# Performance work log

Hardware: AMD Instinct MI355X
Metric: run time of the kernel (lower is better)

The kernel has to match this reference:

```python
import jax, jax.numpy as jnp
import numpy as np

NINPUTS = 16
WIDTH = 128
KSIZE = 21
SPP = 8
BS, CI, H, W = 2, 3, 192, 192
EPS = 1e-08


def _conv(x, w, b, padding):
    y = jax.lax.conv_general_dilated(
        x, w, window_strides=(1, 1), padding=padding,
        dimension_numbers=("NCHW", "OIHW", "NCHW"))
    return y + b[None, :, None, None]


def apply_kernels(kernel, radiance, ksize):
    """Per-pixel predicted-kernel conv: fused gather-multiply-reduce over taps.
    kernel: (bs, ksize^2, kh, kw), radiance: (bs, ci, h, w).
    Replicates torch apply_kernels (normalization='sum') without materializing
    the (bs, ci, kh, kw, ksize^2) unfold tile tensor."""
    bs, k2, kh, kw = kernel.shape
    _, ci, h, w = radiance.shape
    needed = kh + ksize - 1
    if needed > h:
        crop = (needed - h) // 2
        if crop > 0:
            kernel = kernel[:, :, crop:-crop, crop:-crop]
        kh, kw = kernel.shape[2], kernel.shape[3]
    else:
        crop = (h - needed) // 2
        if crop > 0:
            radiance = radiance[:, :, crop:-crop, crop:-crop]
    taps = jnp.arange(k2, dtype=jnp.int32)
    dy = taps // ksize
    dx = taps % ksize

    def body(acc, idx):
        patch = jax.lax.dynamic_slice(radiance, (0, 0, dy[idx], dx[idx]),
                                      (bs, ci, kh, kw))
        kv = jax.lax.dynamic_slice_in_dim(kernel, idx, 1, axis=1)  # (bs,1,kh,kw)
        return acc + kv * patch, None

    acc0 = jnp.zeros((bs, ci, kh, kw), radiance.dtype)
    weighted_sum, _ = jax.lax.scan(body, acc0, taps)
    kernel_sum = jnp.sum(kernel, axis=1, keepdims=True)  # (bs,1,kh,kw)
    return weighted_sum, kernel_sum


def setup_inputs() -> dict:
    key = jax.random.key(0)
    ks = jax.random.split(key, 10)
    s = 0.05
    inp = {
        "features": jax.random.normal(ks[0], (BS, SPP, NINPUTS, H, W), jnp.float32),
        "radiance": jax.random.uniform(ks[1], (BS, SPP, CI, H, W), jnp.float32),
        # recurrent conv processor (simplified main_processor): SAME 3x3 conv
        "w_rnn": jax.random.normal(ks[2], (WIDTH, NINPUTS + WIDTH, 3, 3), jnp.float32) * s,
        "b_rnn": jnp.zeros((WIDTH,), jnp.float32),
        "w_k1": jax.random.normal(ks[3], (WIDTH, WIDTH + NINPUTS, 3, 3), jnp.float32) * s,
        "b_k1": jnp.zeros((WIDTH,), jnp.float32),
        "w_k2": jax.random.normal(ks[4], (WIDTH, WIDTH, 3, 3), jnp.float32) * s,
        "b_k2": jnp.zeros((WIDTH,), jnp.float32),
        "w_k3": jax.random.normal(ks[5], (KSIZE * KSIZE, WIDTH, 3, 3), jnp.float32) * s,
        "b_k3": jnp.zeros((KSIZE * KSIZE,), jnp.float32),
    }
    return inp


def reference(features, radiance, w_rnn, b_rnn, w_k1, b_k1, w_k2, b_k2, w_k3, b_k3):
    bs, spp, ci, h, w = radiance.shape
    lrelu = lambda x: jax.nn.leaky_relu(x, 0.01)
    state = jnp.zeros((bs, WIDTH, h, w), features.dtype)
    unnorm = sumw = max_k = None
    for step in range(spp):
        f = features[:, step]  # (bs, ninputs, h, w)
        rnn = lrelu(_conv(jnp.concatenate([f, state], axis=1), w_rnn, b_rnn, "SAME"))
        state = rnn
        nf = jnp.concatenate([rnn, f], axis=1)  # (bs, width+ninputs, h, w)
        k = lrelu(_conv(nf, w_k1, b_k1, "VALID"))
        k = lrelu(_conv(k, w_k2, b_k2, "VALID"))
        k = _conv(k, w_k3, b_k3, "VALID")  # (bs, ksize^2, h-6, w-6), linear out
        # online-softmax (flash-attention-style) running max/exp rescale
        new_max = jnp.max(k.reshape(bs, -1), axis=1).reshape(bs, 1, 1, 1)
        if step == 0:
            max_k = new_max
        else:
            old_max = max_k
            max_k = jnp.maximum(old_max, new_max)
        kern = jnp.exp(k - max_k)
        ws, ksum = apply_kernels(kern, radiance[:, step], KSIZE)
        if step == 0:
            unnorm, sumw = ws, ksum
        else:
            scale = jnp.exp(old_max - max_k)
            unnorm = unnorm * scale + ws
            sumw = sumw * scale + ksum
    return unnorm / (sumw + EPS)
```

## Files before the change

### kernel.cpp

```cpp
#include <hip/hip_runtime.h>
#include <stdint.h>

typedef _Float16 half8 __attribute__((ext_vector_type(8)));
typedef _Float16 half4 __attribute__((ext_vector_type(4)));
typedef __attribute__((ext_vector_type(8))) short short8;
typedef __attribute__((ext_vector_type(4))) float f32x4;
typedef __attribute__((ext_vector_type(16))) float f32x16;

__device__ __forceinline__ unsigned encf(float x){
  uint32_t u = __float_as_uint(x);
  return (u & 0x80000000u) ? ~u : (u | 0x80000000u);
}
__device__ __forceinline__ float decf(unsigned u){
  uint32_t b = (u & 0x80000000u) ? (u & 0x7FFFFFFFu) : ~u;
  return __uint_as_float(b);
}
__device__ __forceinline__ void gload16(const void* g, void* l){
  __builtin_amdgcn_global_load_lds(
      (const __attribute__((address_space(1))) void*)g,
      (__attribute__((address_space(3))) void*)l, 16, 0, 0);
}

__global__ __launch_bounds__(256) void zero_u32(unsigned* __restrict__ p, int n){
  for (int i = blockIdx.x*256 + threadIdx.x; i < n; i += gridDim.x*256) p[i] = 0u;
}

__global__ __launch_bounds__(256) void pack_w(const float* __restrict__ w, _Float16* __restrict__ wp,
                                              int CO, int CI, int COP, int CINP){
  int idx = blockIdx.x*256 + threadIdx.x;
  int total = 9*COP*CINP;
  if (idx >= total) return;
  int ci = idx % CINP;
  int rest = idx / CINP;
  int co = rest % COP;
  int t  = rest / COP;
  float v = 0.f;
  if (co < CO && ci < CI) v = w[((size_t)co*CI + ci)*9 + t];
  int kc = ci >> 4, chl = ci & 15;
  wp[(((size_t)kc*9 + t)*(COP/32) + (co>>5))*512 + (co&31)*16 + chl] = (_Float16)v;
}

__global__ __launch_bounds__(256) void pack_bias(const float* __restrict__ b, float* __restrict__ bp, int n, int npad){
  int i = blockIdx.x*256 + threadIdx.x;
  if (i < npad) bp[i] = (i < n) ? b[i] : 0.f;
}

__global__ __launch_bounds__(256) void pack_feat(const float* __restrict__ f,
                                                 _Float16* __restrict__ rnn_b,
                                                 _Float16* __restrict__ k1_in,
                                                 unsigned fbstr, unsigned rbstr, unsigned kbstr){
  int p = blockIdx.x*256 + threadIdx.x;
  if (p >= 36864) return;
  int b = blockIdx.y;
  int y = p / 192, x = p % 192;
  const float* fb = f + (size_t)b*fbstr;
  _Float16* r = rnn_b + (size_t)b*rbstr + ((size_t)(y+1)*194 + (x+1))*144;
  _Float16* k = k1_in + (size_t)b*kbstr + (size_t)p*144;
  #pragma unroll
  for (int c = 0; c < 16; ++c){
    _Float16 v = (_Float16)fb[c*36864 + p];
    r[c] = v;
    k[128 + c] = v;
  }
}

template<int CINP, bool RELU, bool K3, bool DUAL>
__global__ __launch_bounds__(128, 2) void conv3(
    const _Float16* __restrict__ X, int Wst, unsigned xbstr,
    const _Float16* __restrict__ Wp, int COP,
    const float* __restrict__ bias,
    _Float16* __restrict__ Y, int Wst_out, int DCP, unsigned ybstr,
    _Float16* __restrict__ Y2, unsigned y2str,
    unsigned* __restrict__ slot, int Ho, int Wo,
    int nco)
{
  constexpr int KC    = CINP/16;
  constexpr int SROWS = K3 ? 10 : 6;
  constexpr int ITEMS = SROWS*34*2;
  constexpr int NRND  = (ITEMS + 127)/128;
  __shared__ _Float16 lds[2][ITEMS*8];

  const int tid  = threadIdx.x;
  const int lane = tid & 63;
  const int wid  = tid >> 6;
  const int l31  = lane & 31;
  const int hsel = lane >> 5;
  const int xb   = blockIdx.x * 32;
  const int yb   = blockIdx.y * (K3 ? 8 : 4);
  const int co_blk = blockIdx.z % nco;
  const int b      = blockIdx.z / nco;

  const _Float16* Xb = X + (size_t)b * xbstr;
  const int NG = COP/32;
  const size_t wtap = (size_t)NG*512;
  const _Float16* wbase = Wp
      + ((size_t)(K3 ? (co_blk*2) : (co_blk*4 + wid*2)))*512 + l31*16 + hsel*8;

  uint32_t goff[NRND];
  #pragma unroll
  for (int k = 0; k < NRND; ++k){
    int item = k*128 + tid;
    if (item < ITEMS){
      int row  = item / 68;
      int rem  = item % 68;
      int col  = rem >> 1;
      int half = rem & 1;
      int pix  = (yb + row)*Wst + xb + col;
      goff[k] = (uint32_t)(((uint32_t)pix*CINP + half*8) * 2);
    } else goff[k] = 0;
  }

  auto stage = [&](int buf, int kc){
    const char* xp = (const char*)Xb + (size_t)kc*32;
    char* lb = (char*)&lds[buf][0];
    #pragma unroll
    for (int k = 0; k < NRND; ++k){
      if (k*128 + tid < ITEMS)
        gload16(xp + goff[k], lb + k*2048 + wid*1024);
    }
  };

  uint32_t boffe[4];
  #pragma unroll
  for (int n = 0; n < 4; ++n){
    const int row = K3 ? (wid*4 + n) : n;
    boffe[n] = (uint32_t)((row*34 + l31)*16 + hsel*8);
  }

  f32x16 acc[4][2] = {};
  half8 wreg[3][2];
  #pragma unroll
  for (int s3 = 0; s3 < 3; ++s3)
    #pragma unroll
    for (int g = 0; g < 2; ++g)
      wreg[s3][g] = *reinterpret_cast<const half8*>(wbase + (size_t)s3*wtap + g*512);

  stage(0, 0);
  __syncthreads();
  for (int kc = 0; kc < KC; ++kc){
    if (kc + 1 < KC) stage((kc+1)&1, kc+1);
    const _Float16* wt = wbase + (size_t)(kc*9)*wtap;
    const _Float16* lb = &lds[kc&1][0];
    half8 breg[2][4];
    #pragma unroll
    for (int n = 0; n < 4; ++n)
      breg[0][n] = *reinterpret_cast<const half8*>(lb + boffe[n]);
    #pragma unroll
    for (int t = 0; t < 9; ++t){
      const int cur = t & 1, nxt = cur ^ 1;
      if (t < 8){
        const int ky1 = (t+1)/3, kx1 = (t+1) - ky1*3;
        #pragma unroll
        for (int n = 0; n < 4; ++n)
          breg[nxt][n] = *reinterpret_cast<const half8*>(lb + boffe[n] + (ky1*34 + kx1)*16);
      }
      #pragma unroll
      for (int n = 0; n < 4; ++n)
        #pragma unroll
        for (int g = 0; g < 2; ++g)
          acc[n][g] = __builtin_amdgcn_mfma_f32_32x32x16_f16(
              wreg[t % 3][g], breg[cur][n], acc[n][g], 0, 0, 0);
      #pragma unroll
      for (int g = 0; g < 2; ++g)
        wreg[t % 3][g] = *reinterpret_cast<const half8*>(wt + (size_t)(t+3)*wtap + g*512);
    }
    if (kc + 1 < KC) __syncthreads();
  }

  const int x = xb + l31;
  float lmax = -3.0e38f;
  #pragma unroll
  for (int n = 0; n < 4; ++n){
    const int y = yb + (K3 ? (wid*4 + n) : n);
    if (y < Ho && x < Wo){
      #pragma unroll
      for (int g = 0; g < 2; ++g){
        #pragma unroll
        for (int q = 0; q < 4; ++q){
          const int cb = (K3 ? (co_blk*64 + g*32) : ((wid*2 + g)*32))
                         + 4*hsel + 8*q;
          f32x4 bs = *reinterpret_cast<const f32x4*>(bias + cb);
          float v[4];
          #pragma unroll
          for (int j = 0; j < 4; ++j){
            float tv = acc[n][g][q*4 + j] + bs[j];
            if (RELU) tv = tv > 0.f ? tv : 0.01f*tv;
            v[j] = tv;
          }
          if constexpr (!K3){
            half4 pk;
            #pragma unroll
            for (int j = 0; j < 4; ++j) pk[j] = (_Float16)v[j];
            *reinterpret_cast<half4*>(Y + (size_t)b*ybstr + ((size_t)y*Wst_out + x)*DCP + cb) = pk;
            if constexpr (DUAL)
              *reinterpret_cast<half4*>(Y2 + (size_t)b*y2str
                  + ((size_t)(y+1)*194 + (x+1))*144 + 16 + cb) = pk;
          } else {
            _Float16* yp = Y + (size_t)b*ybstr;
            #pragma unroll
            for (int j = 0; j < 4; ++j){
              if (cb + j < 441){
                yp[(size_t)(cb+j)*29584 + (size_t)y*172 + x] = (_Float16)v[j];
                lmax = fmaxf(lmax, v[j]);
              }
            }
          }
        }
      }
    }
  }
  if constexpr (K3){
    #pragma unroll
    for (int o = 32; o > 0; o >>= 1) lmax = fmaxf(lmax, __shfl_xor(lmax, o));
    if (lane == 0) atomicMax(slot + b, encf(lmax));
  }
}

__global__ void update_max(float* __restrict__ st, unsigned* __restrict__ slot, int step){
  int b = threadIdx.x;
  if (b < 2){
    float nm   = decf(slot[b]);
    float oldM = st[2*b];
    float M    = (step == 0) ? nm : fmaxf(oldM, nm);
    st[2*b+1] = (step == 0) ? 0.f : expf(oldM - M);
    st[2*b]   = M;
    slot[b] = 0u;
  }
}

__global__ __launch_bounds__(256) void apply_acc(
    const _Float16* __restrict__ k3out, const float* __restrict__ rad,
    const float* __restrict__ st,
    float* __restrict__ unnorm, float* __restrict__ sumw)
{
  const int tx = threadIdx.x & 63, ty = threadIdx.x >> 6;
  const int x = blockIdx.x*64 + tx;
  const int y = blockIdx.y*4 + ty;
  const int b = blockIdx.z;
  if (x >= 172 || y >= 172) return;
  const float M = st[2*b], scale = st[2*b+1];
  const _Float16* kp = k3out + (size_t)b*13046544 + (size_t)y*172 + x;
  const float* rb = rad + (size_t)b*884736;
  float a0 = 0.f, a1 = 0.f, a2 = 0.f, aw = 0.f;
  for (int dy = 0; dy < 21; ++dy){
    const float* r0 = rb + (size_t)(y+dy)*192 + x;
    #pragma unroll
    for (int dx = 0; dx < 21; ++dx){
      float w = __expf((float)kp[(size_t)(dy*21+dx)*29584] - M);
      aw += w;
      a0 += w * r0[dx];
      a1 += w * r0[36864 + dx];
      a2 += w * r0[73728 + dx];
    }
  }
  size_t p = (size_t)b*88752 + (size_t)y*172 + x;
  size_t ps = (size_t)b*29584 + (size_t)y*172 + x;
  unnorm[p]        = unnorm[p]*scale        + a0;
  unnorm[p+29584]  = unnorm[p+29584]*scale  + a1;
  unnorm[p+59168]  = unnorm[p+59168]*scale  + a2;
  sumw[ps]         = sumw[ps]*scale         + aw;
}

__global__ __launch_bounds__(256) void finalize_out(const float* __restrict__ unnorm,
                                                    const float* __restrict__ sumw,
                                                    float* __restrict__ out){
  int i = blockIdx.x*256 + threadIdx.x;
  int b = blockIdx.y;
  if (i >= 88752) return;
  int p = i % 29584;
  out[(size_t)b*88752 + i] = unnorm[(size_t)b*88752 + i] / (sumw[(size_t)b*29584 + p] + 1e-8f);
}

extern "C" void kernel_launch(void* const* d_in, const int* in_sizes, int n_in,
                              void* d_out, int out_size, void* d_ws, size_t ws_size,
                              hipStream_t stream) {
  const float* features = (const float*)d_in[0];
  const float* radiance = (const float*)d_in[1];
  const float* w_rnn = (const float*)d_in[2];
  const float* b_rnn = (const float*)d_in[3];
  const float* w_k1  = (const float*)d_in[4];
  const float* b_k1  = (const float*)d_in[5];
  const float* w_k2  = (const float*)d_in[6];
  const float* b_k2  = (const float*)d_in[7];
  const float* w_k3  = (const float*)d_in[8];
  const float* b_k3  = (const float*)d_in[9];
  float* out = (float*)d_out;

  char* ws = (char*)d_ws;
  size_t off = 0;
  auto alloc = [&](size_t bytes)->char*{
    char* p = ws + off;
    off = (off + bytes + 255) & ~(size_t)255;
    return p;
  };
  const size_t WSLACK = 98304;
  _Float16* wp_rnn   = (_Float16*)alloc((size_t)9*128*144*2 + WSLACK);
  _Float16* wp_k1    = (_Float16*)alloc((size_t)9*128*144*2 + WSLACK);
  _Float16* wp_k2    = (_Float16*)alloc((size_t)9*128*128*2 + WSLACK);
  _Float16* wp_k3    = (_Float16*)alloc((size_t)9*448*128*2 + WSLACK);
  float*    bias_k3p = (float*)   alloc((size_t)448*4);
  const unsigned RB  = 194u*194u*144u;
  const unsigned KB  = (192u*192u+64u)*144u;
  const unsigned K2B = (194u*190u+64u)*128u;
  const unsigned K3B = (194u*188u+64u)*128u;
  const unsigned KOB = 441u*29584u;
  _Float16* rnn_inA = (_Float16*)alloc((size_t)2*RB*2);
  _Float16* rnn_inB = (_Float16*)alloc((size_t)2*RB*2);
  _Float16* k1_in  = (_Float16*)alloc((size_t)2*KB*2);
  _Float16* k2_in  = (_Float16*)alloc((size_t)2*K2B*2);
  _Float16* k3_in  = (_Float16*)alloc((size_t)2*K3B*2);
  _Float16* k3_out = (_Float16*)alloc((size_t)2*KOB*2);
  float*    accz   = (float*)   alloc((size_t)236678*4);
  if (off > ws_size) return;

  float*    unnorm = accz;
  float*    sumw   = accz + 177504;
  float*    st     = accz + 236672;
  unsigned* slot   = (unsigned*)(accz + 236676);

  _Float16* rnn_buf[2] = { rnn_inA, rnn_inB };

  pack_w<<<(9*128*144+255)/256, 256, 0, stream>>>(w_rnn, wp_rnn, 128, 144, 128, 144);
  pack_w<<<(9*128*144+255)/256, 256, 0, stream>>>(w_k1,  wp_k1,  128, 144, 128, 144);
  pack_w<<<(9*128*128+255)/256, 256, 0, stream>>>(w_k2,  wp_k2,  128, 128, 128, 128);
  pack_w<<<(9*448*128+255)/256, 256, 0, stream>>>(w_k3,  wp_k3,  441, 128, 448, 128);
  pack_bias<<<2, 256, 0, stream>>>(b_k3, bias_k3p, 441, 448);

  zero_u32<<<2048, 256, 0, stream>>>((unsigned*)rnn_inA, (int)RB);
  zero_u32<<<2048, 256, 0, stream>>>((unsigned*)rnn_inB, (int)RB);
  zero_u32<<<925,  256, 0, stream>>>((unsigned*)accz, 236678);

  for (int s = 0; s < 8; ++s){
    const float* f   = features + (size_t)s*16*36864;
    const float* rad = radiance + (size_t)s*3*36864;
    _Float16* rcur = rnn_buf[s & 1];
    _Float16* rnxt = rnn_buf[(s + 1) & 1];
    pack_feat<<<dim3(144,2), 256, 0, stream>>>(f, rcur, k1_in,
                                               8u*16u*36864u, RB, KB);
    conv3<144,true ,false,true ><<<dim3(6,48,2), 128, 0, stream>>>(
        rcur, 194, RB, wp_rnn, 128, b_rnn, k1_in, 192, 144, KB,
        rnxt, RB, nullptr, 192, 192, 1);
    conv3<144,true ,false,false><<<dim3(6,45,2), 128, 0, stream>>>(
        k1_in + (size_t)(7*192 + 7)*144, 192, KB, wp_k1, 128, b_k1,
        k2_in + (size_t)(7*190 + 7)*128, 190, 128, K2B,
        nullptr, 0, nullptr, 178, 178, 1);
    conv3<128,true ,false,false><<<dim3(6,44,2), 128, 0, stream>>>(
        k2_in + (size_t)(7*190 + 7)*128, 190, K2B, wp_k2, 128, b_k2,
        k3_in + (size_t)(7*188 + 7)*128, 188, 128, K3B,
        nullptr, 0, nullptr, 174, 174, 1);
    conv3<128,false,true ,false><<<dim3(6,22,14), 128, 0, stream>>>(
        k3_in + (size_t)(7*188 + 7)*128, 188, K3B, wp_k3, 448, bias_k3p,
        k3_out, 0, 0, KOB, nullptr, 0, slot, 172, 172, 7);
    update_max<<<1, 64, 0, stream>>>(st, slot, s);
    apply_acc<<<dim3(3,43,2), 256, 0, stream>>>(k3_out, rad, st, unnorm, sumw);
  }
  finalize_out<<<dim3(347,2), 256, 0, stream>>>(unnorm, sumw, out);
}
```

Before: 2.265 ms.

## Fuse max update into last conv block via ticket; relax inter-chunk barrier

Removes the separate update_max launch by having the last-finishing block of the K3 conv compute the running max and rescale factor, using an atomic ticket counter with threadfences. It also replaces __syncthreads between channel chunks with an explicit s_waitcnt vmcnt(6) plus s_barrier, so some outstanding global loads can stay in flight across the barrier. This saves one tiny kernel launch per step and may shorten barrier stalls. The partial vmcnt wait relies on knowing exactly which loads are outstanding, and if that count is wrong the LDS data may be read before it arrives.

```diff
diff --git a/kernel.cpp b/kernel.cpp
--- a/kernel.cpp
+++ b/kernel.cpp
@@ -71,8 +71,8 @@
     const float* __restrict__ bias,
     _Float16* __restrict__ Y, int Wst_out, int DCP, unsigned ybstr,
     _Float16* __restrict__ Y2, unsigned y2str,
-    unsigned* __restrict__ slot, int Ho, int Wo,
-    int nco)
+    unsigned* __restrict__ slot, float* __restrict__ stt, unsigned* __restrict__ ticket,
+    int step, int Ho, int Wo, int nco)
 {
   constexpr int KC    = CINP/16;
   constexpr int SROWS = K3 ? 10 : 6;
@@ -164,7 +164,9 @@
       for (int g = 0; g < 2; ++g)
         wreg[t % 3][g] = *reinterpret_cast<const half8*>(wt + (size_t)(t+3)*wtap + g*512);
     }
-    if (kc + 1 < KC) __syncthreads();
+    if (kc + 1 < KC){
+      asm volatile("s_waitcnt vmcnt(6)\n\ts_barrier" ::: "memory");
+    }
   }
 
   const int x = xb + l31;
@@ -213,18 +215,25 @@
     #pragma unroll
     for (int o = 32; o > 0; o >>= 1) lmax = fmaxf(lmax, __shfl_xor(lmax, o));
     if (lane == 0) atomicMax(slot + b, encf(lmax));
-  }
-}
-
-__global__ void update_max(float* __restrict__ st, unsigned* __restrict__ slot, int step){
-  int b = threadIdx.x;
-  if (b < 2){
-    float nm   = decf(slot[b]);
-    float oldM = st[2*b];
-    float M    = (step == 0) ? nm : fmaxf(oldM, nm);
-    st[2*b+1] = (step == 0) ? 0.f : expf(oldM - M);
-    st[2*b]   = M;
-    slot[b] = 0u;
+    __syncthreads();
+    if (tid == 0){
+      __threadfence();
+      unsigned total = gridDim.x * gridDim.y * gridDim.z;
+      unsigned prev = atomicAdd(ticket, 1u);
+      if (prev == total - 1u){
+        #pragma unroll
+        for (int b2 = 0; b2 < 2; ++b2){
+          float nm   = decf(slot[b2]);
+          float oldM = stt[2*b2];
+          float M    = (step == 0) ? nm : fmaxf(oldM, nm);
+          stt[2*b2+1] = (step == 0) ? 0.f : expf(oldM - M);
+          stt[2*b2]   = M;
+          slot[b2] = 0u;
+        }
+        __threadfence();
+        *ticket = 0u;
+      }
+    }
   }
 }
 
@@ -310,13 +319,14 @@
   _Float16* k2_in  = (_Float16*)alloc((size_t)2*K2B*2);
   _Float16* k3_in  = (_Float16*)alloc((size_t)2*K3B*2);
   _Float16* k3_out = (_Float16*)alloc((size_t)2*KOB*2);
-  float*    accz   = (float*)   alloc((size_t)236678*4);
+  float*    accz   = (float*)   alloc((size_t)236680*4);
   if (off > ws_size) return;
 
   float*    unnorm = accz;
   float*    sumw   = accz + 177504;
   float*    st     = accz + 236672;
   unsigned* slot   = (unsigned*)(accz + 236676);
+  unsigned* ticket = (unsigned*)(accz + 236678);
 
   _Float16* rnn_buf[2] = { rnn_inA, rnn_inB };
 
@@ -328,7 +338,7 @@
 
   zero_u32<<<2048, 256, 0, stream>>>((unsigned*)rnn_inA, (int)RB);
   zero_u32<<<2048, 256, 0, stream>>>((unsigned*)rnn_inB, (int)RB);
-  zero_u32<<<925,  256, 0, stream>>>((unsigned*)accz, 236678);
+  zero_u32<<<925,  256, 0, stream>>>((unsigned*)accz, 236680);
 
   for (int s = 0; s < 8; ++s){
     const float* f   = features + (size_t)s*16*36864;
@@ -339,19 +349,18 @@
                                                8u*16u*36864u, RB, KB);
     conv3<144,true ,false,true ><<<dim3(6,48,2), 128, 0, stream>>>(
         rcur, 194, RB, wp_rnn, 128, b_rnn, k1_in, 192, 144, KB,
-        rnxt, RB, nullptr, 192, 192, 1);
+        rnxt, RB, nullptr, nullptr, nullptr, 0, 192, 192, 1);
     conv3<144,true ,false,false><<<dim3(6,45,2), 128, 0, stream>>>(
         k1_in + (size_t)(7*192 + 7)*144, 192, KB, wp_k1, 128, b_k1,
         k2_in + (size_t)(7*190 + 7)*128, 190, 128, K2B,
-        nullptr, 0, nullptr, 178, 178, 1);
+        nullptr, 0, nullptr, nullptr, nullptr, 0, 178, 178, 1);
     conv3<128,true ,false,false><<<dim3(6,44,2), 128, 0, stream>>>(
         k2_in + (size_t)(7*190 + 7)*128, 190, K2B, wp_k2, 128, b_k2,
         k3_in + (size_t)(7*188 + 7)*128, 188, 128, K3B,
-        nullptr, 0, nullptr, 174, 174, 1);
+        nullptr, 0, nullptr, nullptr, nullptr, 0, 174, 174, 1);
     conv3<128,false,true ,false><<<dim3(6,22,14), 128, 0, stream>>>(
         k3_in + (size_t)(7*188 + 7)*128, 188, K3B, wp_k3, 448, bias_k3p,
-        k3_out, 0, 0, KOB, nullptr, 0, slot, 172, 172, 7);
-    update_max<<<1, 64, 0, stream>>>(st, slot, s);
+        k3_out, 0, 0, KOB, nullptr, 0, slot, st, ticket, s, 172, 172, 7);
     apply_acc<<<dim3(3,43,2), 256, 0, stream>>>(k3_out, rad, st, unnorm, sumw);
   }
   finalize_out<<<dim3(347,2), 256, 0, stream>>>(unnorm, sumw, out);
```

Result: slower. 2.621 ms (+15.7%).
